# Kernel optimization log

Hardware: AMD Instinct MI355X
Metric: run time of the kernel (lower is better)

The kernel has to match this reference:

```python
import jax, jax.numpy as jnp
import numpy as np

N_QUBITS = 10
EMBED_DIM = 512
FFN_DIM = 2048
DIM = 2 ** N_QUBITS


def _apply_rx(state, theta, wire):
    # state: (N, 2^n) complex64; theta: scalar or (N,)
    N = state.shape[0]
    hi = 2 ** wire                      # dims before the wire axis (wire 0 = MSB)
    lo = 2 ** (N_QUBITS - 1 - wire)
    s = state.reshape(N, hi, 2, lo)
    th = jnp.asarray(theta, jnp.float32).reshape(-1, 1, 1)  # (N,1,1) or (1,1,1)
    c = jnp.cos(th / 2).astype(jnp.complex64)
    ms = (-1j * jnp.sin(th / 2)).astype(jnp.complex64)
    s0, s1 = s[:, :, 0, :], s[:, :, 1, :]
    out = jnp.stack([c * s0 + ms * s1, ms * s0 + c * s1], axis=2)
    return out.reshape(N, DIM)


def _apply_cnot(state, ctrl, tgt):
    N = state.shape[0]
    s = state.reshape((N,) + (2,) * N_QUBITS)
    s0 = jax.lax.index_in_dim(s, 0, axis=ctrl + 1, keepdims=True)
    s1 = jax.lax.index_in_dim(s, 1, axis=ctrl + 1, keepdims=True)
    s1 = jnp.flip(s1, axis=tgt + 1)  # X on target where control == 1
    return jnp.concatenate([s0, s1], axis=ctrl + 1).reshape(N, DIM)


def _pauliz_signs():
    idx = np.arange(DIM)
    bits = (idx[:, None] >> (N_QUBITS - 1 - np.arange(N_QUBITS))[None, :]) & 1
    return jnp.asarray(1.0 - 2.0 * bits, jnp.float32)  # (2^n, n)


def _quantum_layer(tokens, rx_params):
    # tokens: (N, embed_dim); uses first n_qubits features as encoder angles
    N = tokens.shape[0]
    state = jnp.zeros((N, DIM), jnp.complex64).at[:, 0].set(1.0)
    for w in range(N_QUBITS):                    # encoder: RX(x_w) on wire w
        state = _apply_rx(state, tokens[:, w], w)
    for w in range(N_QUBITS):                    # trainable RX per wire
        state = _apply_rx(state, rx_params[w], w)
    for w in range(N_QUBITS - 1):                # CNOT chain
        state = _apply_cnot(state, w, w + 1)
    state = _apply_cnot(state, N_QUBITS - 1, 0)  # wrap-around CNOT
    probs = state.real ** 2 + state.imag ** 2    # (N, 2^n)
    return probs @ _pauliz_signs()               # (N, n_qubits) <Z_w>


def setup_inputs() -> dict:
    key = jax.random.key(0)
    ks = jax.random.split(key, 6)
    x = jax.random.normal(ks[0], (16, 1024, EMBED_DIM), jnp.float32)
    rx_params = jax.random.normal(ks[1], (N_QUBITS,), jnp.float32)
    lim1 = 1.0 / np.sqrt(N_QUBITS)
    w1 = jax.random.uniform(ks[2], (FFN_DIM, N_QUBITS), jnp.float32, -lim1, lim1)
    b1 = jax.random.uniform(ks[3], (FFN_DIM,), jnp.float32, -lim1, lim1)
    lim2 = 1.0 / np.sqrt(FFN_DIM)
    w2 = jax.random.uniform(ks[4], (EMBED_DIM, FFN_DIM), jnp.float32, -lim2, lim2)
    b2 = jax.random.uniform(ks[5], (EMBED_DIM,), jnp.float32, -lim2, lim2)
    return {"x": x, "rx_params": rx_params, "w1": w1, "b1": b1, "w2": w2, "b2": b2}


def reference(x, rx_params, w1, b1, w2, b2):
    B, S, _ = x.shape
    q_out = _quantum_layer(x.reshape(B * S, EMBED_DIM), rx_params)
    q_out = q_out.reshape(B, S, N_QUBITS)
    h = jax.nn.relu(q_out @ w1.T + b1)           # dropout is identity in eval
    return h @ w2.T + b2
```

## Files before the change

### kernel.cpp

```cpp
#include <hip/hip_runtime.h>
#include <hip/hip_bf16.h>
#include <math.h>


typedef __attribute__((ext_vector_type(8))) short short8;
typedef __attribute__((ext_vector_type(8))) unsigned short ushort8;
typedef __attribute__((ext_vector_type(4))) float fx4;

constexpr int EDIM = 512;
constexpr int FDIM = 2048;
constexpr int NQ   = 10;
constexpr int BK   = 32;
constexpr int NCH  = FDIM / BK;

__device__ __forceinline__ ushort f2bf(float f) {
    union { float f; unsigned u; } v; v.f = f;
    unsigned u = v.u + 0x7FFFu + ((v.u >> 16) & 1u);
    return (ushort)(u >> 16);
}
__device__ __forceinline__ unsigned bits2(__hip_bfloat162 h) {
    union { __hip_bfloat162 h; unsigned u; } v; v.h = h; return v.u;
}
__device__ __forceinline__ void gload_lds16(const void* g, void* l) {
    __builtin_amdgcn_global_load_lds(
        (const __attribute__((address_space(1))) void*)g,
        (__attribute__((address_space(3))) void*)l, 16, 0, 0);
}

__global__ void prep(const float* __restrict__ w2, ushort* __restrict__ w2b) {
    int gid = blockIdx.x * blockDim.x + threadIdx.x;
    int np  = gridDim.x * blockDim.x;
    for (int i = gid; i < EDIM * FDIM / 4; i += np) {
        float4 v = ((const float4*)w2)[i];
        ushort4 o; o.x = f2bf(v.x); o.y = f2bf(v.y); o.z = f2bf(v.z); o.w = f2bf(v.w);
        ((ushort4*)w2b)[i] = o;
    }
}

__global__ __launch_bounds__(256, 2) void gemm1(
    const float* __restrict__ x, const float* __restrict__ rx,
    const float* __restrict__ w1, const float* __restrict__ b1,
    ushort* __restrict__ h, int m_base)
{
    __shared__ float qs[32][NQ];
    const int tid = threadIdx.x;
    const int m0  = m_base + blockIdx.x * 32;

    if (tid < 32) {
        const float* xr = x + (size_t)(m0 + tid) * EDIM;
        float c[NQ], q[NQ];
        #pragma unroll
        for (int w = 0; w < NQ; ++w) c[w] = cosf(xr[w] + rx[w]);
        float p0 = c[1];
        #pragma unroll
        for (int w = 2; w < NQ; ++w) p0 *= c[w];
        q[0] = p0;
        float p = c[0];
        #pragma unroll
        for (int w = 1; w < NQ; ++w) { p *= c[w]; q[w] = p; }
        #pragma unroll
        for (int w = 0; w < NQ; ++w) qs[tid][w] = q[w];
    }
    __syncthreads();

    float wv[80];
    {
        const float4* wp = (const float4*)(w1 + (size_t)tid * 80);
        #pragma unroll
        for (int u = 0; u < 20; ++u) ((float4*)wv)[u] = wp[u];
    }
    float bv[8];
    {
        float4 a = *(const float4*)(b1 + tid * 8);
        float4 b = *(const float4*)(b1 + tid * 8 + 4);
        bv[0]=a.x; bv[1]=a.y; bv[2]=a.z; bv[3]=a.w;
        bv[4]=b.x; bv[5]=b.y; bv[6]=b.z; bv[7]=b.w;
    }
    ushort* hrow = h + (size_t)m0 * FDIM + tid * 8;

    for (int m = 0; m < 32; ++m) {
        float qv[NQ];
        #pragma unroll
        for (int w = 0; w < NQ; ++w) qv[w] = qs[m][w];
        float a[8];
        #pragma unroll
        for (int r = 0; r < 8; ++r) a[r] = bv[r];
        #pragma unroll
        for (int w = 0; w < NQ; ++w)
            #pragma unroll
            for (int r = 0; r < 8; ++r)
                a[r] = fmaf(qv[w], wv[r * 10 + w], a[r]);
        ushort8 o;
        #pragma unroll
        for (int r = 0; r < 4; ++r) {
            unsigned p = bits2(__float22bfloat162_rn(
                make_float2(fmaxf(a[2*r], 0.f), fmaxf(a[2*r+1], 0.f))));
            o[2*r]   = (ushort)(p & 0xFFFFu);
            o[2*r+1] = (ushort)(p >> 16);
        }
        *(ushort8*)(hrow + (size_t)m * FDIM) = o;
    }
}

__global__ __launch_bounds__(256, 3) void gemm2(
    const ushort* __restrict__ h,
    const ushort* __restrict__ w2b,
    const float* __restrict__ b2,
    float* __restrict__ out, int m_base)
{
    __shared__ ushort As[128 * BK];
    __shared__ ushort Bs[128 * BK];

    const int tid  = threadIdx.x;
    const int bm   = blockIdx.x >> 2, bn = blockIdx.x & 3;
    const int m0   = m_base + bm * 128, n0 = bn * 128;
    const int wave = tid >> 6, lane = tid & 63;
    const int quad = lane >> 4, l16 = lane & 15;
    const int wm   = wave >> 1, wn = wave & 1;

    const ushort* ga0 = h  + (size_t)(m0 + (tid >> 2)) * FDIM + (tid & 3) * 8;
    const ushort* ga1 = ga0 + (size_t)64 * FDIM;
    const ushort* gb0 = w2b + (size_t)(n0 + (tid >> 2)) * FDIM + (tid & 3) * 8;
    const ushort* gb1 = gb0 + (size_t)64 * FDIM;
    ushort* lA0 = &As[wave * 512];
    ushort* lA1 = &As[2048 + wave * 512];
    ushort* lB0 = &Bs[wave * 512];
    ushort* lB1 = &Bs[2048 + wave * 512];

    const int aro = (wm * 64 + l16) * BK + quad * 8;
    const int bro = (wn * 64 + l16) * BK + quad * 8;

    fx4 acc[4][4];
    #pragma unroll
    for (int a = 0; a < 4; ++a)
        #pragma unroll
        for (int b = 0; b < 4; ++b) acc[a][b] = fx4{0.f, 0.f, 0.f, 0.f};

    for (int i = 0; i < NCH; ++i) {
        gload_lds16(ga0, lA0);  gload_lds16(ga1, lA1);
        gload_lds16(gb0, lB0);  gload_lds16(gb1, lB1);
        ga0 += BK; ga1 += BK; gb0 += BK; gb1 += BK;
        __syncthreads();

        short8 af[4], bf[4];
        #pragma unroll
        for (int mt = 0; mt < 4; ++mt) af[mt] = *(const short8*)&As[aro + mt * 16 * BK];
        #pragma unroll
        for (int nt = 0; nt < 4; ++nt) bf[nt] = *(const short8*)&Bs[bro + nt * 16 * BK];

        #pragma unroll
        for (int mt = 0; mt < 4; ++mt)
            #pragma unroll
            for (int nt = 0; nt < 4; ++nt)
                acc[mt][nt] = __builtin_amdgcn_mfma_f32_16x16x32_bf16(
                    af[mt], bf[nt], acc[mt][nt], 0, 0, 0);
        __syncthreads();
    }

    float bb[4];
    #pragma unroll
    for (int nt = 0; nt < 4; ++nt) bb[nt] = b2[n0 + wn * 64 + nt * 16 + l16];
    #pragma unroll
    for (int mt = 0; mt < 4; ++mt) {
        const int mbase = m0 + wm * 64 + mt * 16 + quad * 4;
        #pragma unroll
        for (int nt = 0; nt < 4; ++nt) {
            const int n = n0 + wn * 64 + nt * 16 + l16;
            #pragma unroll
            for (int r = 0; r < 4; ++r)
                out[(size_t)(mbase + r) * EDIM + n] = acc[mt][nt][r] + bb[nt];
        }
    }
}

extern "C" void kernel_launch(void* const* d_in, const int* in_sizes, int n_in,
                              void* d_out, int out_size, void* d_ws, size_t ws_size,
                              hipStream_t stream) {
    const float* x  = (const float*)d_in[0];
    const float* rx = (const float*)d_in[1];
    const float* w1 = (const float*)d_in[2];
    const float* b1 = (const float*)d_in[3];
    const float* w2 = (const float*)d_in[4];
    const float* b2 = (const float*)d_in[5];
    float* out = (float*)d_out;

    const int M = in_sizes[0] / EDIM;

    const size_t w2bytes = (size_t)EDIM * FDIM * 2;
    ushort* w2b = (ushort*)d_ws;
    ushort* h   = (ushort*)((char*)d_ws + w2bytes);

    int Ms = M;
    {
        size_t avail = (ws_size > w2bytes) ? ws_size - w2bytes : 0;
        int cap = (int)(avail / ((size_t)FDIM * 2));
        cap &= ~127;
        if (cap < 128) cap = 128;
        if (Ms > cap) Ms = cap;
    }

    hipLaunchKernelGGL(prep, dim3(256), dim3(256), 0, stream, w2, w2b);

    for (int mb = 0; mb < M; mb += Ms) {
        int cur = (M - mb < Ms) ? (M - mb) : Ms;
        hipLaunchKernelGGL(gemm1, dim3(cur / 32), dim3(256), 0, stream,
                           x, rx, w1, b1, h, mb);
        hipLaunchKernelGGL(gemm2, dim3((cur / 128) * 4), dim3(256), 0, stream,
                           h, w2b, b2, out, mb);
    }
}
```

Baseline: 154.1 us.

## Double K-tile depth in gemm2 with XOR-swizzled LDS layout and 2D grid

Raises the gemm2 K-chunk from 32 to 64, which halves the number of barrier-separated iterations. The LDS tiles now use an XOR swizzle on the 16-byte blocks so that the wider rows avoid bank conflicts on fragment reads. The grid becomes 2D with blockIdx.y selecting the N tile, which changes block rasterization so that consecutive blocks share N instead of M. The cost is a doubled LDS footprint and an occupancy hint lowered from 3 to 2 blocks per CU.

```diff
diff --git a/kernel.cpp b/kernel.cpp
--- a/kernel.cpp
+++ b/kernel.cpp
@@ -10,7 +10,7 @@
 constexpr int EDIM = 512;
 constexpr int FDIM = 2048;
 constexpr int NQ   = 10;
-constexpr int BK   = 32;
+constexpr int BK   = 64;
 constexpr int NCH  = FDIM / BK;
 
 __device__ __forceinline__ ushort f2bf(float f) {
@@ -102,7 +102,7 @@
     }
 }
 
-__global__ __launch_bounds__(256, 3) void gemm2(
+__global__ __launch_bounds__(256, 2) void gemm2(
     const ushort* __restrict__ h,
     const ushort* __restrict__ w2b,
     const float* __restrict__ b2,
@@ -112,23 +112,32 @@
     __shared__ ushort Bs[128 * BK];
 
     const int tid  = threadIdx.x;
-    const int bm   = blockIdx.x >> 2, bn = blockIdx.x & 3;
+    const int bm   = blockIdx.x;
+    const int bn   = blockIdx.y;
     const int m0   = m_base + bm * 128, n0 = bn * 128;
     const int wave = tid >> 6, lane = tid & 63;
     const int quad = lane >> 4, l16 = lane & 15;
     const int wm   = wave >> 1, wn = wave & 1;
 
-    const ushort* ga0 = h  + (size_t)(m0 + (tid >> 2)) * FDIM + (tid & 3) * 8;
-    const ushort* ga1 = ga0 + (size_t)64 * FDIM;
-    const ushort* gb0 = w2b + (size_t)(n0 + (tid >> 2)) * FDIM + (tid & 3) * 8;
-    const ushort* gb1 = gb0 + (size_t)64 * FDIM;
-    ushort* lA0 = &As[wave * 512];
-    ushort* lA1 = &As[2048 + wave * 512];
-    ushort* lB0 = &Bs[wave * 512];
-    ushort* lB1 = &Bs[2048 + wave * 512];
-
-    const int aro = (wm * 64 + l16) * BK + quad * 8;
-    const int bro = (wn * 64 + l16) * BK + quad * 8;
+    const int srow0 = tid >> 3;
+    const int sbs   = tid & 7;
+    const ushort* gA[4]; const ushort* gB[4];
+    #pragma unroll
+    for (int u = 0; u < 4; ++u) {
+        int row = u * 32 + srow0;
+        int bl  = sbs ^ (row & 7);
+        gA[u] = h   + (size_t)(m0 + row) * FDIM + bl * 8;
+        gB[u] = w2b + (size_t)(n0 + row) * FDIM + bl * 8;
+    }
+    const int ldst = wave * 512;
+
+    const int swz = l16 & 7;
+    int aro[4], bro[4];
+    #pragma unroll
+    for (int t = 0; t < 4; ++t) {
+        aro[t] = (wm * 64 + t * 16 + l16) * BK;
+        bro[t] = (wn * 64 + t * 16 + l16) * BK;
+    }
 
     fx4 acc[4][4];
     #pragma unroll
@@ -137,23 +146,32 @@
         for (int b = 0; b < 4; ++b) acc[a][b] = fx4{0.f, 0.f, 0.f, 0.f};
 
     for (int i = 0; i < NCH; ++i) {
-        gload_lds16(ga0, lA0);  gload_lds16(ga1, lA1);
-        gload_lds16(gb0, lB0);  gload_lds16(gb1, lB1);
-        ga0 += BK; ga1 += BK; gb0 += BK; gb1 += BK;
+        #pragma unroll
+        for (int u = 0; u < 4; ++u) {
+            gload_lds16(gA[u], &As[u * 2048 + ldst]);
+            gload_lds16(gB[u], &Bs[u * 2048 + ldst]);
+            gA[u] += BK; gB[u] += BK;
+        }
         __syncthreads();
 
-        short8 af[4], bf[4];
-        #pragma unroll
-        for (int mt = 0; mt < 4; ++mt) af[mt] = *(const short8*)&As[aro + mt * 16 * BK];
-        #pragma unroll
-        for (int nt = 0; nt < 4; ++nt) bf[nt] = *(const short8*)&Bs[bro + nt * 16 * BK];
-
-        #pragma unroll
-        for (int mt = 0; mt < 4; ++mt)
-            #pragma unroll
-            for (int nt = 0; nt < 4; ++nt)
-                acc[mt][nt] = __builtin_amdgcn_mfma_f32_16x16x32_bf16(
-                    af[mt], bf[nt], acc[mt][nt], 0, 0, 0);
+        short8 af[4][2], bf[4][2];
+        #pragma unroll
+        for (int t = 0; t < 4; ++t)
+            #pragma unroll
+            for (int hf = 0; hf < 2; ++hf) {
+                const int blk = (hf * 4 + quad) ^ swz;
+                af[t][hf] = *(const short8*)&As[aro[t] + blk * 8];
+                bf[t][hf] = *(const short8*)&Bs[bro[t] + blk * 8];
+            }
+
+        #pragma unroll
+        for (int hf = 0; hf < 2; ++hf)
+            #pragma unroll
+            for (int mt = 0; mt < 4; ++mt)
+                #pragma unroll
+                for (int nt = 0; nt < 4; ++nt)
+                    acc[mt][nt] = __builtin_amdgcn_mfma_f32_16x16x32_bf16(
+                        af[mt][hf], bf[nt][hf], acc[mt][nt], 0, 0, 0);
         __syncthreads();
     }
 
@@ -205,7 +223,7 @@
         int cur = (M - mb < Ms) ? (M - mb) : Ms;
         hipLaunchKernelGGL(gemm1, dim3(cur / 32), dim3(256), 0, stream,
                            x, rx, w1, b1, h, mb);
-        hipLaunchKernelGGL(gemm2, dim3((cur / 128) * 4), dim3(256), 0, stream,
+        hipLaunchKernelGGL(gemm2, dim3(cur / 128, 4), dim3(256), 0, stream,
                            h, w2b, b2, out, mb);
     }
 }
```

Result: faster. 139.9 us (-9.2%).
